# Performance work log

Measured on AMD Instinct MI355X. Metric: run time of the kernel, lower is better.

The kernel has to match this reference:

```python
import jax, jax.numpy as jnp
import numpy as np

ALPHA = 0.2          # LeakyReLU negative slope
ORTHO_LAMBDA = 0.01  # orthogonal regularization weight


def setup_inputs() -> dict:
    key = jax.random.key(0)
    ks = jax.random.split(key, 9)
    N, IN, OUT, NR, H = 50000, 128, 128, 64, 4
    E1, E2 = 200000, 50000
    return {
        "input": jax.random.normal(ks[0], (N, IN), jnp.float32),
        "edge": jax.random.randint(ks[1], (2, E1), 0, N),
        "edge_embed": jax.random.normal(ks[2], (E1, NR), jnp.float32),
        "edge_list_nhop": jax.random.randint(ks[3], (2, E2), 0, N),
        "edge_embed_nhop": jax.random.normal(ks[4], (E2, NR), jnp.float32),
        "proj": jax.random.normal(ks[5], (H, IN, IN), jnp.float32) / np.sqrt(IN).astype(np.float32),
        "W": jax.random.normal(ks[6], (H, OUT, 2 * IN + NR), jnp.float32) * 0.08,
        "a": jax.random.normal(ks[7], (H, 1, OUT), jnp.float32) * 0.1,
        "head_weights": jnp.ones((H,), jnp.float32),
    }


def reference(input, edge, edge_embed, edge_list_nhop, edge_embed_nhop, proj, W, a, head_weights):
    N, IN = input.shape
    H, OUT, _ = W.shape
    e = jnp.concatenate([edge, edge_list_nhop], axis=1)              # [2, E]
    emb = jnp.concatenate([edge_embed, edge_embed_nhop], axis=0)     # [E, NR]
    src, tgt = e[0], e[1]

    # per-head orthogonal projections: head_input[h] = input @ proj[h].T -> [H, N, IN]
    hin = jnp.einsum('ni,hoi->hno', input, proj)

    # edge_m = W @ concat(h_src, h_tgt, rel) without materializing the concat
    W_src, W_tgt, W_rel = W[:, :, :IN], W[:, :, IN:2 * IN], W[:, :, 2 * IN:]
    edge_m = (jnp.einsum('hei,hoi->heo', hin[:, src, :], W_src)
              + jnp.einsum('hei,hoi->heo', hin[:, tgt, :], W_tgt)
              + jnp.einsum('er,hor->heo', emb, W_rel))               # [H, E, OUT]

    scores = jnp.einsum('heo,ho->he', edge_m, a[:, 0, :])            # [H, E]
    powers = -jnp.where(scores > 0, scores, ALPHA * scores)         # -leakyrelu
    edge_e = jnp.exp(powers)                                         # [H, E]

    seg = lambda v: jax.ops.segment_sum(v, src, num_segments=N)
    e_rowsum = jnp.clip(jax.vmap(seg)(edge_e), 1e-12, None)          # [H, N]

    edge_w = edge_e[:, :, None] * edge_m                             # [H, E, OUT]
    head_out = jax.vmap(seg)(edge_w)                                 # [H, N, OUT]

    w = jax.nn.softmax(head_weights)
    out = jnp.einsum('h,hnd->nd', w, head_out)                       # [N, OUT]
    # faithful to torch: divides by the LAST head's e_rowsum (loop leakage)
    out = out / e_rowsum[-1][:, None]

    pp = jnp.einsum('hij,hkj->hik', proj, proj)                      # proj @ proj.T
    eye = jnp.eye(proj.shape[1], dtype=proj.dtype)
    orth_reg = ORTHO_LAMBDA * jnp.sum(jnp.sqrt(jnp.sum((pp - eye) ** 2, axis=(1, 2))))

    return jax.nn.elu(out), orth_reg
```

## Files before the change

### kernel.cpp

```cpp
#include <hip/hip_runtime.h>
#include <math.h>


#define NHEAD 4

typedef unsigned short u16;
typedef __attribute__((ext_vector_type(4))) unsigned short u16x4;
typedef __attribute__((ext_vector_type(8))) unsigned short u16x8;
typedef __attribute__((ext_vector_type(8))) short bf16x8;
typedef __attribute__((ext_vector_type(4))) float f32x4;

__device__ __forceinline__ float bf2f(u16 v) {
    union { unsigned u; float f; } x; x.u = ((unsigned)v) << 16; return x.f;
}
__device__ __forceinline__ u16 f2bf(float f) {
    union { float f; unsigned u; } x; x.f = f;
    const unsigned r = x.u + 0x7FFFu + ((x.u >> 16) & 1u);
    return (u16)(r >> 16);
}

__global__ __launch_bounds__(256) void k1_prep(
    const float* __restrict__ proj, const float* __restrict__ W,
    const float* __restrict__ a, const float* __restrict__ hw,
    u16* __restrict__ M_bf,
    float* __restrict__ asrc, float* __restrict__ atgt, float* __restrict__ arel,
    u16* __restrict__ WcatT_bf, float* __restrict__ wsoft,
    float* __restrict__ orth_part)
{
    __shared__ float projS[128*132];
    __shared__ float WS[32*132];
    __shared__ float tS[128];
    __shared__ float red[256];
    const int h = blockIdx.x;
    const int part = blockIdx.y;
    const int z = blockIdx.z;
    const int tid = threadIdx.x;
    const float* projH = proj + h*(128*128);
    const float* WH = W + h*(128*320);
    const float* aH = a + h*128;

    {
        const float4* p4 = (const float4*)projH;
        for (int idx = tid; idx < 4096; idx += 256)
            *(float4*)&projS[(idx>>5)*132 + (idx&31)*4] = p4[idx];
    }

    if (part < 2) {
        const int koff = part ? 128 : 0;
        for (int idx = tid; idx < 1024; idx += 256) {
            const int ol = idx>>5, jq = idx&31;
            *(float4*)&WS[ol*132 + jq*4] = *(const float4*)&WH[(z*32+ol)*320 + koff + jq*4];
        }
        __syncthreads();
        u16* Mout = M_bf + ((size_t)(part*4 + h))*16384;
        for (int idx = tid; idx < 1024; idx += 256) {
            const int ol = idx>>5, jq = idx&31;
            float4 acc; acc.x=0.f; acc.y=0.f; acc.z=0.f; acc.w=0.f;
            for (int i = 0; i < 128; ++i) {
                const float wv = WS[ol*132 + i];
                const float4 pv = *(const float4*)&projS[i*132 + jq*4];
                acc.x += wv*pv.x; acc.y += wv*pv.y; acc.z += wv*pv.z; acc.w += wv*pv.w;
            }
            u16x4 pk; pk.x=f2bf(acc.x); pk.y=f2bf(acc.y); pk.z=f2bf(acc.z); pk.w=f2bf(acc.w);
            *(u16x4*)&Mout[(z*32+ol)*128 + jq*4] = pk;
        }
        if (z == 0) {
            if (tid < 128) {
                float s = 0.f;
                for (int o = 0; o < 128; ++o) s += aH[o]*WH[o*320 + koff + tid];
                tS[tid] = s;
            }
            __syncthreads();
            if (tid < 128) {
                float s = 0.f;
                for (int i = 0; i < 128; ++i) s += tS[i]*projS[i*132 + tid];
                (part ? atgt : asrc)[h*128 + tid] = s;
            }
        }
    } else {
        __syncthreads();
        float local = 0.f;
        const int base = z*4096;
        for (int idx = base + tid; idx < base + 4096; idx += 256) {
            const int i = idx>>7, k = idx&127;
            float s = 0.f;
            for (int q = 0; q < 32; ++q) {
                const float4 pi = *(const float4*)&projS[i*132 + q*4];
                const float4 pk = *(const float4*)&projS[k*132 + q*4];
                s += pi.x*pk.x + pi.y*pk.y + pi.z*pk.z + pi.w*pk.w;
            }
            if (i == k) s -= 1.f;
            local += s*s;
        }
        red[tid] = local;
        __syncthreads();
        for (int st = 128; st > 0; st >>= 1) {
            if (tid < st) red[tid] += red[tid+st];
            __syncthreads();
        }
        if (tid == 0) atomicAdd(&orth_part[h], red[0]);
        if (z == 0) {
            if (tid < 64) {
                float s = 0.f;
                for (int o = 0; o < 128; ++o) s += aH[o]*WH[o*320 + 256 + tid];
                arel[h*64 + tid] = s;
            }
            for (int idx = tid; idx < 8192; idx += 256) {
                const int r = idx & 63, o = idx >> 6;
                WcatT_bf[(size_t)o*256 + h*64 + r] = f2bf(WH[o*320 + 256 + r]);
            }
            if (h == 0 && tid == 0) {
                const float m = fmaxf(fmaxf(hw[0],hw[1]), fmaxf(hw[2],hw[3]));
                const float e0=expf(hw[0]-m), e1=expf(hw[1]-m), e2=expf(hw[2]-m), e3=expf(hw[3]-m);
                const float s = e0+e1+e2+e3;
                wsoft[0]=e0/s; wsoft[1]=e1/s; wsoft[2]=e2/s; wsoft[3]=e3/s;
            }
        }
    }
}

__global__ __launch_bounds__(256) void k0_nodes(
    const float* __restrict__ input, const float* __restrict__ asrc, const float* __restrict__ atgt,
    u16* __restrict__ in_bf, float* __restrict__ s_src, float* __restrict__ s_tgt, int N)
{
    __shared__ float aS[512], tS[512];
    const int tid = threadIdx.x;
    for (int idx = tid; idx < 512; idx += 256) { aS[idx] = asrc[idx]; tS[idx] = atgt[idx]; }
    __syncthreads();
    const int n = blockIdx.x*256 + tid;
    if (n >= N) return;
    const float4* inr = (const float4*)(input + (size_t)n*128);
    u16* ob = in_bf + (size_t)n*128;
    float ss[4] = {0.f,0.f,0.f,0.f}, st[4] = {0.f,0.f,0.f,0.f};
    for (int q = 0; q < 32; ++q) {
        const float4 v = inr[q];
        u16x4 pk; pk.x=f2bf(v.x); pk.y=f2bf(v.y); pk.z=f2bf(v.z); pk.w=f2bf(v.w);
        *(u16x4*)(ob + q*4) = pk;
        #pragma unroll
        for (int hh = 0; hh < 4; ++hh) {
            const float4 av = *(const float4*)&aS[hh*128 + q*4];
            const float4 tv = *(const float4*)&tS[hh*128 + q*4];
            ss[hh] += v.x*av.x + v.y*av.y + v.z*av.z + v.w*av.w;
            st[hh] += v.x*tv.x + v.y*tv.y + v.z*tv.z + v.w*tv.w;
        }
    }
    float4 o1; o1.x=ss[0]; o1.y=ss[1]; o1.z=ss[2]; o1.w=ss[3];
    float4 o2; o2.x=st[0]; o2.y=st[1]; o2.z=st[2]; o2.w=st[3];
    *(float4*)(s_src + (size_t)n*4) = o1;
    *(float4*)(s_tgt + (size_t)n*4) = o2;
}

__global__ __launch_bounds__(256) void k2_mfma(
    const u16* __restrict__ in_bf, const u16* __restrict__ M_bf,
    u16* __restrict__ tbl, int N)
{
    __shared__ u16 MS[16384];
    __shared__ u16 DS[128*136];
    const int tid = threadIdx.x;
    const int w = tid >> 6, lane = tid & 63;
    const int bid = blockIdx.x;
    const int nx = gridDim.x >> 3;
    const int swz = (bid & 7)*nx + (bid >> 3);
    const int n0 = (swz >> 3)*256;
    const int mat = swz & 7;
    const int m = lane & 15, kg = lane >> 4;

    {
        const u16* Mp = M_bf + (size_t)mat*16384;
        for (int c = tid; c < 2048; c += 256) {
            const int row = c >> 4, c16 = c & 15;
            const u16x8 v = *(const u16x8*)(Mp + row*128 + c16*8);
            *(u16x8*)((char*)MS + row*256 + ((c16*16) ^ ((row&7)<<4))) = v;
        }
    }
    bf16x8 fa[4][4];
    #pragma unroll
    for (int rt = 0; rt < 4; ++rt) {
        int row = n0 + w*64 + rt*16 + m; if (row >= N) row = N-1;
        const u16* ap = in_bf + (size_t)row*128 + kg*8;
        #pragma unroll
        for (int ks = 0; ks < 4; ++ks) fa[rt][ks] = *(const bf16x8*)(ap + ks*32);
    }
    __syncthreads();

    f32x4 acc[4][8];
    #pragma unroll
    for (int rt = 0; rt < 4; ++rt)
        #pragma unroll
        for (int nt = 0; nt < 8; ++nt) { acc[rt][nt][0]=0.f; acc[rt][nt][1]=0.f; acc[rt][nt][2]=0.f; acc[rt][nt][3]=0.f; }

    #pragma unroll
    for (int nt = 0; nt < 8; ++nt) {
        const int o = nt*16 + m;
        bf16x8 fb[4];
        #pragma unroll
        for (int ks = 0; ks < 4; ++ks) {
            const int c16 = kg + 4*ks;
            fb[ks] = *(const bf16x8*)((const char*)MS + o*256 + ((c16*16) ^ ((o&7)<<4)));
        }
        #pragma unroll
        for (int rt = 0; rt < 4; ++rt)
            #pragma unroll
            for (int ks = 0; ks < 4; ++ks)
                acc[rt][nt] = __builtin_amdgcn_mfma_f32_16x16x32_bf16(fa[rt][ks], fb[ks], acc[rt][nt], 0, 0, 0);
    }

    for (int p = 0; p < 2; ++p) {
        __syncthreads();
        if ((w >> 1) == p) {
            #pragma unroll
            for (int rt = 0; rt < 4; ++rt) {
                const int r0 = (w&1)*64 + rt*16 + kg*4;
                #pragma unroll
                for (int nt = 0; nt < 8; ++nt) {
                    const int o = nt*16 + m;
                    #pragma unroll
                    for (int r = 0; r < 4; ++r)
                        DS[(r0+r)*136 + o] = f2bf(acc[rt][nt][r]);
                }
            }
        }
        __syncthreads();
        for (int idx = tid; idx < 2048; idx += 256) {
            const int row = idx >> 4, seg = idx & 15;
            const int n = n0 + p*128 + row;
            if (n < N) {
                const bf16x8 v = *(const bf16x8*)&DS[row*136 + seg*8];
                *(bf16x8*)(tbl + (size_t)n*1024 + mat*128 + seg*8) = v;
            }
        }
    }
}

__global__ __launch_bounds__(256) void k3_edges(
    const int* __restrict__ edge, const int* __restrict__ nhop,
    const float* __restrict__ emb1, const float* __restrict__ emb2,
    const float* __restrict__ s_src, const float* __restrict__ s_tgt,
    const float* __restrict__ arel,
    float* __restrict__ edge_e, int* __restrict__ deg,
    u16* __restrict__ emb_bf, int E1, int E2)
{
    const int tid = threadIdx.x;
    const int g = tid >> 4, l = tid & 15;
    const int E = E1 + E2;
    const float4 ar0 = *(const float4*)(arel + 0*64 + l*4);
    const float4 ar1 = *(const float4*)(arel + 1*64 + l*4);
    const float4 ar2 = *(const float4*)(arel + 2*64 + l*4);
    const float4 ar3 = *(const float4*)(arel + 3*64 + l*4);
    const int ebase = blockIdx.x*256;
    #pragma unroll 4
    for (int it = 0; it < 16; ++it) {
        const int e = ebase + it*16 + g;
        if (e >= E) continue;
        const float4 v = (e < E1) ? *(const float4*)(emb1 + (size_t)e*64 + l*4)
                                  : *(const float4*)(emb2 + (size_t)(e-E1)*64 + l*4);
        u16x4 pk; pk.x=f2bf(v.x); pk.y=f2bf(v.y); pk.z=f2bf(v.z); pk.w=f2bf(v.w);
        *(u16x4*)(emb_bf + (size_t)e*64 + l*4) = pk;
        float p0 = v.x*ar0.x + v.y*ar0.y + v.z*ar0.z + v.w*ar0.w;
        float p1 = v.x*ar1.x + v.y*ar1.y + v.z*ar1.z + v.w*ar1.w;
        float p2 = v.x*ar2.x + v.y*ar2.y + v.z*ar2.z + v.w*ar2.w;
        float p3 = v.x*ar3.x + v.y*ar3.y + v.z*ar3.z + v.w*ar3.w;
        #pragma unroll
        for (int d = 1; d < 16; d <<= 1) {
            p0 += __shfl_xor(p0, d);
            p1 += __shfl_xor(p1, d);
            p2 += __shfl_xor(p2, d);
            p3 += __shfl_xor(p3, d);
        }
        if (l == 0) {
            int src, tgt;
            if (e < E1) { src = edge[e]; tgt = edge[E1+e]; }
            else { const int e2 = e-E1; src = nhop[e2]; tgt = nhop[E2+e2]; }
            const float4 s4 = *(const float4*)(s_src + (size_t)src*4);
            const float4 t4 = *(const float4*)(s_tgt + (size_t)tgt*4);
            float4 eo;
            { const float sc = s4.x+t4.x+p0; eo.x = expf(sc>0.f ? -sc : -0.2f*sc); }
            { const float sc = s4.y+t4.y+p1; eo.y = expf(sc>0.f ? -sc : -0.2f*sc); }
            { const float sc = s4.z+t4.z+p2; eo.z = expf(sc>0.f ? -sc : -0.2f*sc); }
            { const float sc = s4.w+t4.w+p3; eo.w = expf(sc>0.f ? -sc : -0.2f*sc); }
            *(float4*)(edge_e + (size_t)e*4) = eo;
            atomicAdd(&deg[src], 1);
        }
    }
}

__global__ __launch_bounds__(1024) void k_scanA(const int* __restrict__ deg, int* __restrict__ offsets,
                                                int* __restrict__ bsum, int N)
{
    __shared__ int wsumS[16];
    const int tid = threadIdx.x;
    const int lane = tid & 63, wid = tid >> 6;
    const int i0 = blockIdx.x*4096 + tid*4;
    int a0=0,a1=0,a2=0,a3=0;
    if (i0 + 3 < N) { const int4 t = *(const int4*)(deg + i0); a0=t.x; a1=t.y; a2=t.z; a3=t.w; }
    else { if (i0 < N) a0=deg[i0]; if (i0+1 < N) a1=deg[i0+1]; if (i0+2 < N) a2=deg[i0+2]; }
    const int s1=a0+a1, s2=s1+a2, s3=s2+a3;
    int s = s3;
    #pragma unroll
    for (int d = 1; d < 64; d <<= 1) { const int t = __shfl_up(s, d); if (lane >= d) s += t; }
    if (lane == 63) wsumS[wid] = s;
    __syncthreads();
    if (tid < 16) {
        int t = wsumS[tid];
        #pragma unroll
        for (int d = 1; d < 16; d <<= 1) { const int u = __shfl_up(t, d); if (tid >= d) t += u; }
        wsumS[tid] = t;
    }
    __syncthreads();
    const int ex = (wid ? wsumS[wid-1] : 0) + s - s3;
    if (i0 < N)     offsets[i0]   = ex;
    if (i0+1 < N)   offsets[i0+1] = ex + a0;
    if (i0+2 < N)   offsets[i0+2] = ex + s1;
    if (i0+3 < N)   offsets[i0+3] = ex + s2;
    if (tid == 0) bsum[blockIdx.x] = wsumS[15];
}

__global__ __launch_bounds__(64) void k_scanB(const int* __restrict__ bsum, int* __restrict__ boff,
                                              int* __restrict__ offsets, int nb, int N)
{
    const int tid = threadIdx.x;
    const int v = (tid < nb) ? bsum[tid] : 0;
    int s = v;
    #pragma unroll
    for (int d = 1; d < 64; d <<= 1) { const int t = __shfl_up(s, d); if (tid >= d) s += t; }
    if (tid < nb) boff[tid] = s - v;
    if (tid == 63) offsets[N] = s;
}

__global__ __launch_bounds__(256) void k_fill(
    const int* __restrict__ edge, const int* __restrict__ nhop,
    const float* __restrict__ edge_e,
    const int* __restrict__ offsets, const int* __restrict__ boff, int* __restrict__ cursor,
    int* __restrict__ csr_e, int* __restrict__ csr_tgt, float* __restrict__ ee_perm,
    int E1, int E2)
{
    const int E = E1+E2;
    const int e = blockIdx.x*256 + threadIdx.x;
    if (e >= E) return;
    int src, tgt;
    if (e < E1) { src = edge[e]; tgt = edge[E1+e]; }
    else { const int e2 = e-E1; src = nhop[e2]; tgt = nhop[E2+e2]; }
    const int pos = atomicAdd(&cursor[src], 1);
    const int p = offsets[src] + boff[src>>12] + pos;
    csr_e[p] = e;
    csr_tgt[p] = tgt;
    *(float4*)(ee_perm + (size_t)p*4) = *(const float4*)(edge_e + (size_t)e*4);
}

__global__ __launch_bounds__(256) void k4_gather(
    const float* __restrict__ ee_perm, const int* __restrict__ offsets, const int* __restrict__ boff,
    const int* __restrict__ csr_e, const int* __restrict__ csr_tgt,
    const u16* __restrict__ emb_bf, const u16* __restrict__ tbl,
    const float* __restrict__ wsoft,
    u16* __restrict__ pout_bf, u16* __restrict__ semb_bf, float* __restrict__ rowsum3,
    int N)
{
    const int lane = threadIdx.x & 63;
    const int n = blockIdx.x*4 + (threadIdx.x >> 6);
    if (n >= N) return;
    const int hl = lane >> 4;
    const int hoff = hl*128 + (lane & 15)*8;

    union HT { u16x8 v; unsigned u[4]; };

    float acc[8];
    #pragma unroll
    for (int j = 0; j < 8; ++j) acc[j] = 0.f;
    float sm0=0.f, sm1=0.f, sm2=0.f, sm3=0.f;
    float rsl0=0.f, rsl1=0.f, rsl2=0.f, rsl3=0.f;

    const int start = offsets[n] + boff[n>>12];
    const int end = (n+1 == N) ? offsets[N] : (offsets[n+1] + boff[(n+1)>>12]);
    for (int cb = start; cb < end; cb += 64) {
        const int rem = end - cb;
        const int cnt = rem < 64 ? rem : 64;
        int eL = 0, tgtL = 0;
        float4 eeL; eeL.x=0.f; eeL.y=0.f; eeL.z=0.f; eeL.w=0.f;
        if (lane < cnt) {
            eL   = csr_e[cb + lane];
            tgtL = csr_tgt[cb + lane];
            eeL  = *(const float4*)(ee_perm + (size_t)(cb + lane)*4);
        }
        rsl0 += eeL.x; rsl1 += eeL.y; rsl2 += eeL.z; rsl3 += eeL.w;
        const int cp = (cnt + 3) & ~3;

        HT zz; zz.u[0]=0u; zz.u[1]=0u; zz.u[2]=0u; zz.u[3]=0u;
        HT ht0=zz, ht1=zz, ht2=zz, ht3=zz;
        u16 em0=0, em1=0, em2=0, em3=0;
#define K4_FETCH(J, IDX) { const int tg_ = __shfl(tgtL, (IDX)); const int eg_ = __shfl(eL, (IDX)); \
            ht##J.v = *(const u16x8*)(tbl + (size_t)tg_*1024 + 512 + hoff); \
            em##J = emb_bf[(size_t)eg_*64 + lane]; }
        if (0 < cnt) K4_FETCH(0, 0)
        if (1 < cnt) K4_FETCH(1, 1)
        if (2 < cnt) K4_FETCH(2, 2)
        if (3 < cnt) K4_FETCH(3, 3)

#define K4_STAGE(J) { \
            const float e0 = __shfl(eeL.x, i+J); \
            const float e1 = __shfl(eeL.y, i+J); \
            const float e2 = __shfl(eeL.z, i+J); \
            const float e3 = __shfl(eeL.w, i+J); \
            const float eh = (hl==0)?e0:(hl==1)?e1:(hl==2)?e2:e3; \
            _Pragma("unroll") \
            for (int p = 0; p < 4; ++p) { \
                union{unsigned u; float f;} lo_, hi_; \
                lo_.u = ht##J.u[p] << 16; hi_.u = ht##J.u[p] & 0xffff0000u; \
                acc[2*p]   += eh*lo_.f; \
                acc[2*p+1] += eh*hi_.f; \
            } \
            const float ev = bf2f(em##J); \
            sm0 += e0*ev; sm1 += e1*ev; sm2 += e2*ev; sm3 += e3*ev; \
            { const int ii = i + 4 + J; if (ii < cnt) K4_FETCH(J, ii) } }

        for (int i = 0; i < cp; i += 4) {
            K4_STAGE(0)
            K4_STAGE(1)
            K4_STAGE(2)
            K4_STAGE(3)
        }
#undef K4_STAGE
#undef K4_FETCH
    }

    #pragma unroll
    for (int d = 1; d < 64; d <<= 1) {
        rsl0 += __shfl_xor(rsl0, d);
        rsl1 += __shfl_xor(rsl1, d);
        rsl2 += __shfl_xor(rsl2, d);
        rsl3 += __shfl_xor(rsl3, d);
    }
    {
        const float rsh = (hl==0)?rsl0:(hl==1)?rsl1:(hl==2)?rsl2:rsl3;
        HT hs; hs.v = *(const u16x8*)(tbl + (size_t)n*1024 + hoff);
        #pragma unroll
        for (int p = 0; p < 4; ++p) {
            union{unsigned u; float f;} lo_, hi_;
            lo_.u = hs.u[p] << 16; hi_.u = hs.u[p] & 0xffff0000u;
            acc[2*p]   += rsh*lo_.f;
            acc[2*p+1] += rsh*hi_.f;
        }
    }
    if (lane == 0) rowsum3[n] = fmaxf(rsl3, 1e-12f);

    const float4 ws4 = *(const float4*)wsoft;
    const float wh = (hl==0)?ws4.x:(hl==1)?ws4.y:(hl==2)?ws4.z:ws4.w;
    float p[8];
    #pragma unroll
    for (int j = 0; j < 8; ++j) {
        float pv = wh*acc[j];
        pv += __shfl_xor(pv, 16);
        pv += __shfl_xor(pv, 32);
        p[j] = pv;
    }
    if (hl == 0) {
        u16 pk[8];
        #pragma unroll
        for (int j = 0; j < 8; ++j) pk[j] = f2bf(p[j]);
        *(u16x8*)(pout_bf + (size_t)n*128 + (lane & 15)*8) = *(u16x8*)pk;
    }
    u16* so = semb_bf + (size_t)n*256;
    so[lane]       = f2bf(ws4.x*sm0);
    so[64 + lane]  = f2bf(ws4.y*sm1);
    so[128 + lane] = f2bf(ws4.z*sm2);
    so[192 + lane] = f2bf(ws4.w*sm3);
}

__global__ __launch_bounds__(256) void k5_gemm(
    const u16* __restrict__ semb_bf, const u16* __restrict__ wcatT_bf,
    const u16* __restrict__ pout_bf,
    const float* __restrict__ rowsum3, const float* __restrict__ orth_part,
    float* __restrict__ out, int N)
{
    __shared__ float DS[64*132];
    const int tid = threadIdx.x;
    if (blockIdx.x == 0 && tid == 0)
        out[(size_t)N*128] = 0.01f*(sqrtf(orth_part[0])+sqrtf(orth_part[1])+sqrtf(orth_part[2])+sqrtf(orth_part[3]));
    const int w = tid >> 6, lane = tid & 63;
    const int m = lane & 15, kg = lane >> 4;
    const int n0 = blockIdx.x*64;

    bf16x8 fa[8];
    {
        int row = n0 + w*16 + m; if (row >= N) row = N-1;
        const u16* ap = semb_bf + (size_t)row*256 + kg*8;
        #pragma unroll
        for (int ks = 0; ks < 8; ++ks) fa[ks] = *(const bf16x8*)(ap + ks*32);
    }
    f32x4 acc[8];
    #pragma unroll
    for (int nt = 0; nt < 8; ++nt) { acc[nt][0]=0.f; acc[nt][1]=0.f; acc[nt][2]=0.f; acc[nt][3]=0.f; }
    #pragma unroll
    for (int nt = 0; nt < 8; ++nt) {
        const u16* bp = wcatT_bf + (size_t)(nt*16 + m)*256 + kg*8;
        #pragma unroll
        for (int ks = 0; ks < 8; ++ks) {
            const bf16x8 fb = *(const bf16x8*)(bp + ks*32);
            acc[nt] = __builtin_amdgcn_mfma_f32_16x16x32_bf16(fa[ks], fb, acc[nt], 0, 0, 0);
        }
    }
    #pragma unroll
    for (int nt = 0; nt < 8; ++nt) {
        const int o = nt*16 + m;
        const int r0 = w*16 + kg*4;
        #pragma unroll
        for (int r = 0; r < 4; ++r)
            DS[(r0+r)*132 + o] = acc[nt][r];
    }
    __syncthreads();
    for (int idx = tid; idx < 2048; idx += 256) {
        const int row = idx >> 5, q = idx & 31;
        const int n = n0 + row;
        if (n < N) {
            const float4 d = *(const float4*)&DS[row*132 + q*4];
            const u16x4 pb = *(const u16x4*)(pout_bf + (size_t)n*128 + q*4);
            const float rinv = 1.0f / rowsum3[n];
            float v0 = (bf2f(pb.x) + d.x)*rinv;
            float v1 = (bf2f(pb.y) + d.y)*rinv;
            float v2 = (bf2f(pb.z) + d.z)*rinv;
            float v3 = (bf2f(pb.w) + d.w)*rinv;
            v0 = (v0 > 0.f) ? v0 : expm1f(v0);
            v1 = (v1 > 0.f) ? v1 : expm1f(v1);
            v2 = (v2 > 0.f) ? v2 : expm1f(v2);
            v3 = (v3 > 0.f) ? v3 : expm1f(v3);
            float4 r4; r4.x=v0; r4.y=v1; r4.z=v2; r4.w=v3;
            *(float4*)(out + (size_t)n*128 + q*4) = r4;
        }
    }
}

extern "C" void kernel_launch(void* const* d_in, const int* in_sizes, int n_in,
                              void* d_out, int out_size, void* d_ws, size_t ws_size,
                              hipStream_t stream)
{
    const float* input = (const float*)d_in[0];
    const int*   edge  = (const int*)d_in[1];
    const float* emb1  = (const float*)d_in[2];
    const int*   nhop  = (const int*)d_in[3];
    const float* emb2  = (const float*)d_in[4];
    const float* proj  = (const float*)d_in[5];
    const float* W     = (const float*)d_in[6];
    const float* a     = (const float*)d_in[7];
    const float* hw    = (const float*)d_in[8];
    float* out = (float*)d_out;

    const int N  = in_sizes[0] / 128;
    const int E1 = in_sizes[1] / 2;
    const int E2 = in_sizes[3] / 2;
    const int E  = E1 + E2;
    (void)n_in; (void)out_size; (void)ws_size;

    char* wsb = (char*)d_ws;
    size_t off = 0;
    auto alloc = [&](size_t bytes) -> char* {
        char* p = wsb + off;
        off += (bytes + 255) & ~(size_t)255;
        return p;
    };
    u16*   in_bf    = (u16*)alloc((size_t)N*128*2);
    u16*   tbl      = (u16*)alloc((size_t)N*1024*2);
    u16*   semb_bf  = (u16*)alloc((size_t)N*256*2);
    u16*   pout_bf  = (u16*)alloc((size_t)N*128*2);
    u16*   emb_bf   = (u16*)alloc((size_t)E*64*2);
    float* edge_e   = (float*)alloc((size_t)E*4*4);
    float* ee_perm  = (float*)alloc((size_t)E*4*4);
    int*   csr_e    = (int*)alloc((size_t)E*4);
    int*   csr_tgt  = (int*)alloc((size_t)E*4);
    u16*   M_bf     = (u16*)alloc((size_t)8*16384*2);
    u16*   WcatT_bf = (u16*)alloc((size_t)128*256*2);
    float* asrc     = (float*)alloc(512*4);
    float* atgt     = (float*)alloc(512*4);
    float* arel     = (float*)alloc(256*4);
    float* s_src    = (float*)alloc((size_t)N*4*4);
    float* s_tgt    = (float*)alloc((size_t)N*4*4);
    float* wsoft    = (float*)alloc(4*4);
    float* rowsum3  = (float*)alloc((size_t)N*4);
    int*   offsets  = (int*)alloc((size_t)(N+1)*4);
    int*   bsum     = (int*)alloc(64*4);
    int*   boff     = (int*)alloc(64*4);
    const size_t zoff0 = off;
    float* orth_part= (float*)alloc(4*4);
    int*   deg      = (int*)alloc((size_t)N*4);
    int*   cursor   = (int*)alloc((size_t)N*4);
    const size_t zoff1 = off;

    hipMemsetAsync(wsb + zoff0, 0, zoff1 - zoff0, stream);

    const int nbScan = (N + 4095) / 4096;
    const int nx = (N + 255) / 256;

    k1_prep<<<dim3(NHEAD,3,4), dim3(256), 0, stream>>>(proj, W, a, hw, M_bf,
                                                       asrc, atgt, arel, WcatT_bf, wsoft, orth_part);
    k0_nodes<<<dim3((N+255)/256), dim3(256), 0, stream>>>(input, asrc, atgt, in_bf, s_src, s_tgt, N);
    k2_mfma<<<dim3(nx*8), dim3(256), 0, stream>>>(in_bf, M_bf, tbl, N);
    k3_edges<<<dim3((E+255)/256), dim3(256), 0, stream>>>(edge, nhop, emb1, emb2, s_src, s_tgt,
                                                          arel, edge_e, deg, emb_bf, E1, E2);
    k_scanA<<<dim3(nbScan), dim3(1024), 0, stream>>>(deg, offsets, bsum, N);
    k_scanB<<<dim3(1), dim3(64), 0, stream>>>(bsum, boff, offsets, nbScan, N);
    k_fill<<<dim3((E+255)/256), dim3(256), 0, stream>>>(edge, nhop, edge_e, offsets, boff, cursor,
                                                        csr_e, csr_tgt, ee_perm, E1, E2);
    k4_gather<<<dim3((N+3)/4), dim3(256), 0, stream>>>(ee_perm, offsets, boff, csr_e, csr_tgt, emb_bf,
                                                       tbl, wsoft, pout_bf, semb_bf, rowsum3, N);
    k5_gemm<<<dim3((N+63)/64), dim3(256), 0, stream>>>(semb_bf, WcatT_bf, pout_bf, rowsum3, orth_part,
                                                       out, N);
}
```

Measured before the change: 272.8 us.

## Drop LDS staging in MFMA table kernel, use LDS broadcast in gather, halve orth work

The k2 MFMA kernel stops staging the projection matrix and output tile through shared memory. It keeps the weight fragments in registers, processes node rows in 16-row subtiles, and stores bf16 results directly using packed convert instructions. The k4 gather kernel replaces cross-lane shuffles of edge weights, targets and edge ids with per-wave shared-memory buffers. The orthogonality term in k1 computes only the upper triangle of P·Pᵀ (doubling off-diagonal terms) and spreads it over more blocks, with the extra blocks in the other branches returning early. The trade-off is higher register pressure and uncoalesced narrow global stores in k2, plus LDS traffic in k4's inner loop.

```diff
diff --git a/kernel.cpp b/kernel.cpp
--- a/kernel.cpp
+++ b/kernel.cpp
@@ -35,6 +35,7 @@
     const int part = blockIdx.y;
     const int z = blockIdx.z;
     const int tid = threadIdx.x;
+    if (part < 2 && z >= 4) return;
     const float* projH = proj + h*(128*128);
     const float* WH = W + h*(128*320);
     const float* aH = a + h*128;
@@ -80,17 +81,18 @@
     } else {
         __syncthreads();
         float local = 0.f;
-        const int base = z*4096;
-        for (int idx = base + tid; idx < base + 4096; idx += 256) {
+        const int base = z*2048;
+        for (int idx = base + tid; idx < base + 2048; idx += 256) {
             const int i = idx>>7, k = idx&127;
+            if (i > k) continue;
             float s = 0.f;
             for (int q = 0; q < 32; ++q) {
                 const float4 pi = *(const float4*)&projS[i*132 + q*4];
                 const float4 pk = *(const float4*)&projS[k*132 + q*4];
                 s += pi.x*pk.x + pi.y*pk.y + pi.z*pk.z + pi.w*pk.w;
             }
-            if (i == k) s -= 1.f;
-            local += s*s;
+            if (i == k) { s -= 1.f; local += s*s; }
+            else local += 2.f*s*s;
         }
         red[tid] = local;
         __syncthreads();
@@ -154,8 +156,6 @@
     const u16* __restrict__ in_bf, const u16* __restrict__ M_bf,
     u16* __restrict__ tbl, int N)
 {
-    __shared__ u16 MS[16384];
-    __shared__ u16 DS[128*136];
     const int tid = threadIdx.x;
     const int w = tid >> 6, lane = tid & 63;
     const int bid = blockIdx.x;
@@ -165,68 +165,39 @@
     const int mat = swz & 7;
     const int m = lane & 15, kg = lane >> 4;
 
-    {
-        const u16* Mp = M_bf + (size_t)mat*16384;
-        for (int c = tid; c < 2048; c += 256) {
-            const int row = c >> 4, c16 = c & 15;
-            const u16x8 v = *(const u16x8*)(Mp + row*128 + c16*8);
-            *(u16x8*)((char*)MS + row*256 + ((c16*16) ^ ((row&7)<<4))) = v;
-        }
-    }
-    bf16x8 fa[4][4];
-    #pragma unroll
-    for (int rt = 0; rt < 4; ++rt) {
-        int row = n0 + w*64 + rt*16 + m; if (row >= N) row = N-1;
-        const u16* ap = in_bf + (size_t)row*128 + kg*8;
-        #pragma unroll
-        for (int ks = 0; ks < 4; ++ks) fa[rt][ks] = *(const bf16x8*)(ap + ks*32);
-    }
-    __syncthreads();
-
-    f32x4 acc[4][8];
-    #pragma unroll
-    for (int rt = 0; rt < 4; ++rt)
-        #pragma unroll
-        for (int nt = 0; nt < 8; ++nt) { acc[rt][nt][0]=0.f; acc[rt][nt][1]=0.f; acc[rt][nt][2]=0.f; acc[rt][nt][3]=0.f; }
-
-    #pragma unroll
-    for (int nt = 0; nt < 8; ++nt) {
-        const int o = nt*16 + m;
+    const u16* Mp = M_bf + (size_t)mat*16384;
+    bf16x8 fa[8][4];
+    #pragma unroll
+    for (int nt = 0; nt < 8; ++nt)
+        #pragma unroll
+        for (int ks = 0; ks < 4; ++ks)
+            fa[nt][ks] = *(const bf16x8*)(Mp + (nt*16 + m)*128 + ks*32 + kg*8);
+
+    #pragma unroll
+    for (int sub = 0; sub < 4; ++sub) {
+        const int nrow = n0 + w*64 + sub*16 + m;
+        const int nclamp = (nrow < N) ? nrow : (N-1);
         bf16x8 fb[4];
         #pragma unroll
-        for (int ks = 0; ks < 4; ++ks) {
-            const int c16 = kg + 4*ks;
-            fb[ks] = *(const bf16x8*)((const char*)MS + o*256 + ((c16*16) ^ ((o&7)<<4)));
-        }
-        #pragma unroll
-        for (int rt = 0; rt < 4; ++rt)
+        for (int ks = 0; ks < 4; ++ks)
+            fb[ks] = *(const bf16x8*)(in_bf + (size_t)nclamp*128 + ks*32 + kg*8);
+        f32x4 acc[8];
+        #pragma unroll
+        for (int nt = 0; nt < 8; ++nt) { acc[nt][0]=0.f; acc[nt][1]=0.f; acc[nt][2]=0.f; acc[nt][3]=0.f; }
+        #pragma unroll
+        for (int nt = 0; nt < 8; ++nt)
             #pragma unroll
             for (int ks = 0; ks < 4; ++ks)
-                acc[rt][nt] = __builtin_amdgcn_mfma_f32_16x16x32_bf16(fa[rt][ks], fb[ks], acc[rt][nt], 0, 0, 0);
-    }
-
-    for (int p = 0; p < 2; ++p) {
-        __syncthreads();
-        if ((w >> 1) == p) {
+                acc[nt] = __builtin_amdgcn_mfma_f32_16x16x32_bf16(fa[nt][ks], fb[ks], acc[nt], 0, 0, 0);
+        if (nrow < N) {
+            u16* dst = tbl + (size_t)nrow*1024 + mat*128 + kg*4;
             #pragma unroll
-            for (int rt = 0; rt < 4; ++rt) {
-                const int r0 = (w&1)*64 + rt*16 + kg*4;
-                #pragma unroll
-                for (int nt = 0; nt < 8; ++nt) {
-                    const int o = nt*16 + m;
-                    #pragma unroll
-                    for (int r = 0; r < 4; ++r)
-                        DS[(r0+r)*136 + o] = f2bf(acc[rt][nt][r]);
-                }
-            }
-        }
-        __syncthreads();
-        for (int idx = tid; idx < 2048; idx += 256) {
-            const int row = idx >> 4, seg = idx & 15;
-            const int n = n0 + p*128 + row;
-            if (n < N) {
-                const bf16x8 v = *(const bf16x8*)&DS[row*136 + seg*8];
-                *(bf16x8*)(tbl + (size_t)n*1024 + mat*128 + seg*8) = v;
+            for (int nt = 0; nt < 8; ++nt) {
+                unsigned lo, hi;
+                asm("v_cvt_pk_bf16_f32 %0, %1, %2" : "=v"(lo) : "v"(acc[nt][0]), "v"(acc[nt][1]));
+                asm("v_cvt_pk_bf16_f32 %0, %1, %2" : "=v"(hi) : "v"(acc[nt][2]), "v"(acc[nt][3]));
+                uint2 pk; pk.x = lo; pk.y = hi;
+                *(uint2*)(dst + nt*16) = pk;
             }
         }
     }
@@ -355,8 +326,11 @@
     u16* __restrict__ pout_bf, u16* __restrict__ semb_bf, float* __restrict__ rowsum3,
     int N)
 {
+    __shared__ float eeS[4][64][4];
+    __shared__ int   tgeS[4][64][2];
     const int lane = threadIdx.x & 63;
-    const int n = blockIdx.x*4 + (threadIdx.x >> 6);
+    const int wv = threadIdx.x >> 6;
+    const int n = blockIdx.x*4 + wv;
     if (n >= N) return;
     const int hl = lane >> 4;
     const int hoff = hl*128 + (lane & 15)*8;
@@ -382,12 +356,15 @@
             eeL  = *(const float4*)(ee_perm + (size_t)(cb + lane)*4);
         }
         rsl0 += eeL.x; rsl1 += eeL.y; rsl2 += eeL.z; rsl3 += eeL.w;
+        *(float4*)&eeS[wv][lane][0] = eeL;
+        tgeS[wv][lane][0] = tgtL;
+        tgeS[wv][lane][1] = eL;
         const int cp = (cnt + 3) & ~3;
 
         HT zz; zz.u[0]=0u; zz.u[1]=0u; zz.u[2]=0u; zz.u[3]=0u;
         HT ht0=zz, ht1=zz, ht2=zz, ht3=zz;
         u16 em0=0, em1=0, em2=0, em3=0;
-#define K4_FETCH(J, IDX) { const int tg_ = __shfl(tgtL, (IDX)); const int eg_ = __shfl(eL, (IDX)); \
+#define K4_FETCH(J, IDX) { const int tg_ = tgeS[wv][IDX][0]; const int eg_ = tgeS[wv][IDX][1]; \
             ht##J.v = *(const u16x8*)(tbl + (size_t)tg_*1024 + 512 + hoff); \
             em##J = emb_bf[(size_t)eg_*64 + lane]; }
         if (0 < cnt) K4_FETCH(0, 0)
@@ -396,11 +373,8 @@
         if (3 < cnt) K4_FETCH(3, 3)
 
 #define K4_STAGE(J) { \
-            const float e0 = __shfl(eeL.x, i+J); \
-            const float e1 = __shfl(eeL.y, i+J); \
-            const float e2 = __shfl(eeL.z, i+J); \
-            const float e3 = __shfl(eeL.w, i+J); \
-            const float eh = (hl==0)?e0:(hl==1)?e1:(hl==2)?e2:e3; \
+            const float4 ee4 = *(const float4*)&eeS[wv][i+J][0]; \
+            const float eh = eeS[wv][i+J][hl]; \
             _Pragma("unroll") \
             for (int p = 0; p < 4; ++p) { \
                 union{unsigned u; float f;} lo_, hi_; \
@@ -409,7 +383,7 @@
                 acc[2*p+1] += eh*hi_.f; \
             } \
             const float ev = bf2f(em##J); \
-            sm0 += e0*ev; sm1 += e1*ev; sm2 += e2*ev; sm3 += e3*ev; \
+            sm0 += ee4.x*ev; sm1 += ee4.y*ev; sm2 += ee4.z*ev; sm3 += ee4.w*ev; \
             { const int ii = i + 4 + J; if (ii < cnt) K4_FETCH(J, ii) } }
 
         for (int i = 0; i < cp; i += 4) {
@@ -588,7 +562,7 @@
     const int nbScan = (N + 4095) / 4096;
     const int nx = (N + 255) / 256;
 
-    k1_prep<<<dim3(NHEAD,3,4), dim3(256), 0, stream>>>(proj, W, a, hw, M_bf,
+    k1_prep<<<dim3(NHEAD,3,8), dim3(256), 0, stream>>>(proj, W, a, hw, M_bf,
                                                        asrc, atgt, arel, WcatT_bf, wsoft, orth_part);
     k0_nodes<<<dim3((N+255)/256), dim3(256), 0, stream>>>(input, asrc, atgt, in_bf, s_src, s_tgt, N);
     k2_mfma<<<dim3(nx*8), dim3(256), 0, stream>>>(in_bf, M_bf, tbl, N);
```

Result: slower. 279.9 us (+2.6%).
